# Kernel tuning notes

Hardware: AMD Instinct MI355X
Metric: run time of the kernel (lower is better)

The kernel has to match this reference:

```python
import jax, jax.numpy as jnp
import numpy as np

B, N, H, E, A, V, L = 64, 196, 512, 512, 512, 20000, 20


def setup_inputs() -> dict:
    key = jax.random.key(0)
    ks = jax.random.split(key, 16)
    s = lambda *sh: 0.02
    return {
        "encoder_outputs": jax.random.normal(ks[0], (B, N, H), dtype=jnp.float32),
        "captions": jax.random.randint(ks[1], (B, L), 0, V, dtype=jnp.int64),
        "emb": jax.random.normal(ks[2], (V, E), dtype=jnp.float32) * 0.02,
        "W_ih": jax.random.normal(ks[3], (4 * H, E + H), dtype=jnp.float32) * 0.02,
        "W_hh": jax.random.normal(ks[4], (4 * H, H), dtype=jnp.float32) * 0.02,
        "b_ih": jax.random.normal(ks[5], (4 * H,), dtype=jnp.float32) * 0.02,
        "b_hh": jax.random.normal(ks[6], (4 * H,), dtype=jnp.float32) * 0.02,
        "enc_W": jax.random.normal(ks[7], (A, H), dtype=jnp.float32) * 0.02,
        "enc_b": jax.random.normal(ks[8], (A,), dtype=jnp.float32) * 0.02,
        "dec_W": jax.random.normal(ks[9], (A, H), dtype=jnp.float32) * 0.02,
        "dec_b": jax.random.normal(ks[10], (A,), dtype=jnp.float32) * 0.02,
        "energy_W": jax.random.normal(ks[11], (1, A), dtype=jnp.float32) * 0.02,
        "energy_b": jax.random.normal(ks[12], (1,), dtype=jnp.float32) * 0.02,
        "fc_W": jax.random.normal(ks[13], (V, H), dtype=jnp.float32) * 0.02,
        "fc_b": jax.random.normal(ks[14], (V,), dtype=jnp.float32) * 0.02,
    }


def reference(encoder_outputs, captions, emb, W_ih, W_hh, b_ih, b_hh,
              enc_W, enc_b, dec_W, dec_b, energy_W, energy_b, fc_W, fc_b):
    b, max_len = captions.shape
    hid = W_hh.shape[1]
    vocab = fc_W.shape[0]
    dt = encoder_outputs.dtype

    # encoder projection is hidden-state independent: hoist out of the loop
    enc_proj = jnp.einsum('bnh,ah->bna', encoder_outputs, enc_W) + enc_b  # [B,N,A]
    # teacher forcing ratio = 1.0 => input at step t is captions[:, t-1]
    emb_seq = emb[captions[:, :-1]]                                      # [B,L-1,E]
    emb_seq = jnp.swapaxes(emb_seq, 0, 1)                                # [L-1,B,E]

    def step(carry, x_t):
        h, c = carry
        dec = h @ dec_W.T + dec_b                                        # [B,A]
        scores = jnp.tanh(enc_proj + dec[:, None, :]) @ energy_W[0] + energy_b[0]  # [B,N]
        attw = jax.nn.softmax(scores, axis=1)
        context = jnp.einsum('bn,bnh->bh', attw, encoder_outputs)        # [B,H]
        lstm_in = jnp.concatenate([x_t, context], axis=1)                # [B,E+H]
        gates = lstm_in @ W_ih.T + b_ih + h @ W_hh.T + b_hh              # [B,4H]
        i, f, g, o = jnp.split(gates, 4, axis=1)
        c_new = jax.nn.sigmoid(f) * c + jax.nn.sigmoid(i) * jnp.tanh(g)
        h_new = jax.nn.sigmoid(o) * jnp.tanh(c_new)
        out = h_new @ fc_W.T + fc_b                                      # [B,V]
        return (h_new, c_new), out

    h0 = jnp.zeros((b, hid), dtype=dt)
    c0 = jnp.zeros((b, hid), dtype=dt)
    (_, _), outs = jax.lax.scan(step, (h0, c0), emb_seq)                 # [L-1,B,V]
    outputs = jnp.concatenate(
        [jnp.zeros((b, 1, vocab), dtype=dt), jnp.swapaxes(outs, 0, 1)], axis=1)
    return outputs
```

## Files before the change

kernel.cpp:

```cpp
#include <hip/hip_runtime.h>
#include <hip/hip_bf16.h>
#include <math.h>

#define B   64
#define NN  196
#define HH  512
#define EE  512
#define AA  512
#define VV  20000
#define LL  20

typedef __attribute__((ext_vector_type(8))) short bf16x8;
typedef __attribute__((ext_vector_type(4))) float floatx4;

__device__ __forceinline__ float tanh_fast(float x) {
  float e2 = __expf(2.f * x);
  return 1.f - 2.f / (e2 + 1.f);
}
__device__ __forceinline__ float sigmoid_fast(float x) {
  return 1.f / (1.f + __expf(-x));
}
__device__ __forceinline__ float bf2f(unsigned short u) {
  return __uint_as_float(((unsigned)u) << 16);
}
__device__ __forceinline__ unsigned short f2bf(float v) {
  __hip_bfloat16 h = __float2bfloat16(v);
  return *reinterpret_cast<unsigned short*>(&h);
}

__device__ __forceinline__ int ldsw(int row, int q4) {
  return (row * 4 + (q4 ^ ((row >> 1) & 3))) * 8;
}
__device__ __forceinline__ int ldsw8(int row, int q8) {
  return (row * 8 + (q8 ^ (row & 7))) * 8;
}

__global__ __launch_bounds__(256) void gemm_mfma_bt(
    const unsigned short* __restrict__ Xb, const unsigned short* __restrict__ Wb,
    const float* __restrict__ bias, float* __restrict__ C,
    int M, int N, int K, int lda, int ldC, int outMode, int gridMX) {
  __shared__ unsigned short As[128 * 32];
  __shared__ unsigned short Bs[128 * 32];
  const int tid = threadIdx.x;
  const int lane = tid & 63;
  const int l15 = lane & 15;
  const int q = lane >> 4;
  const int wv = tid >> 6;
  const int wm = (wv >> 1) * 64;
  const int wn = (wv & 1) * 64;
  int mBase, nBase;
  if (gridMX == 2) {
    const int MT = (M + 127) >> 7, NT = (N + 127) >> 7;
    int wg = blockIdx.x;
    int xcd = wg & 7, idx = wg >> 3;
    int kk = idx / MT, mi = idx - kk * MT;
    int p = kk * 8 + xcd;
    if (p >= NT) return;
    mBase = mi * 128;
    nBase = p * 128;
  } else {
    mBase = blockIdx.y * 128;
    nBase = blockIdx.x * 128;
  }

  const int c0 = tid, c1 = tid + 256;
  const int r0 = c0 >> 2, q0 = c0 & 3;
  const int r1 = c1 >> 2, q1 = c1 & 3;
  const int s0 = ldsw(r0, q0), s1 = ldsw(r1, q1);

  floatx4 zero = {0.f, 0.f, 0.f, 0.f};
  floatx4 acc[4][4];
#pragma unroll
  for (int i = 0; i < 4; ++i)
#pragma unroll
    for (int j = 0; j < 4; ++j) acc[i][j] = zero;

  for (int k0 = 0; k0 < K; k0 += 32) {
    uint4 a0 = *(const uint4*)(Xb + (size_t)(mBase + r0) * lda + k0 + q0 * 8);
    uint4 a1 = *(const uint4*)(Xb + (size_t)(mBase + r1) * lda + k0 + q1 * 8);
    uint4 b0 = *(const uint4*)(Wb + (size_t)(nBase + r0) * K + k0 + q0 * 8);
    uint4 b1 = *(const uint4*)(Wb + (size_t)(nBase + r1) * K + k0 + q1 * 8);
    __syncthreads();
    *(uint4*)&As[s0] = a0;
    *(uint4*)&As[s1] = a1;
    *(uint4*)&Bs[s0] = b0;
    *(uint4*)&Bs[s1] = b1;
    __syncthreads();
    bf16x8 af[4], bfv[4];
#pragma unroll
    for (int i = 0; i < 4; ++i)
      af[i] = *(const bf16x8*)&As[ldsw(wm + i * 16 + l15, q)];
#pragma unroll
    for (int j = 0; j < 4; ++j)
      bfv[j] = *(const bf16x8*)&Bs[ldsw(wn + j * 16 + l15, q)];
#pragma unroll
    for (int i = 0; i < 4; ++i)
#pragma unroll
      for (int j = 0; j < 4; ++j)
        acc[i][j] = __builtin_amdgcn_mfma_f32_16x16x32_bf16(af[i], bfv[j],
                                                            acc[i][j], 0, 0, 0);
  }

#pragma unroll
  for (int i = 0; i < 4; ++i) {
#pragma unroll
    for (int j = 0; j < 4; ++j) {
#pragma unroll
      for (int p = 0; p < 4; ++p) {
        int m = mBase + wm + i * 16 + q * 4 + p;
        int n = nBase + wn + j * 16 + l15;
        if (m < M && n < N) {
          float v = acc[i][j][p];
          if (bias) v += bias[n];
          if (outMode == 1) {
            size_t idx = (size_t)(m & 63) * ((size_t)LL * VV) +
                         (size_t)((m >> 6) + 1) * VV + n;
            C[idx] = v;
          } else if (outMode == 2) {
            ((unsigned short*)C)[(size_t)m * ldC + n] = f2bf(v);
          } else {
            C[(size_t)m * ldC + n] = v;
          }
        }
      }
    }
  }
}

__global__ __launch_bounds__(512) void fused_step(
    const unsigned short* __restrict__ enc_projb,
    const unsigned short* __restrict__ encOutb,
    const unsigned short* __restrict__ dec_Wp,
    const float* __restrict__ dec_b, const float* __restrict__ eW,
    const float* __restrict__ eb,
    const unsigned short* __restrict__ Wgi,
    const float* __restrict__ gx,
    float* __restrict__ c,
    unsigned short* __restrict__ xcur,
    unsigned short* __restrict__ xnxt,
    unsigned short* __restrict__ hb_slot,
    int* __restrict__ flags, int target) {
  const int tid = threadIdx.x;

  if (blockIdx.x < 64) {
    const int b = blockIdx.x;
    __shared__ float hs[512];
    __shared__ float sdec[512];
    __shared__ float sw[NN];
    __shared__ float tmp[256];
    __shared__ float cp[1024];

    hs[tid] = bf2f(xcur[(size_t)b * 1024 + tid]);
    __syncthreads();
    {
      float dacc = dec_b[tid];
#pragma unroll 4
      for (int kg = 0; kg < 64; ++kg) {
        bf16x8 w8 = *(const bf16x8*)(dec_Wp + (size_t)((kg << 9) + tid) * 8);
#pragma unroll
        for (int j = 0; j < 8; ++j)
          dacc += hs[kg * 8 + j] * bf2f((unsigned short)w8[j]);
      }
      sdec[tid] = dacc;
    }
    __syncthreads();

    int wvv = tid >> 6, lane = tid & 63;
    float ew8[8], sd8[8];
#pragma unroll
    for (int j = 0; j < 8; ++j) {
      ew8[j] = eW[lane * 8 + j];
      sd8[j] = sdec[lane * 8 + j];
    }
    float eb0 = eb[0];
    for (int n = wvv; n < NN; n += 8) {
      const unsigned short* ep =
          enc_projb + ((size_t)b * NN + n) * 512 + lane * 8;
      bf16x8 v8 = *(const bf16x8*)ep;
      float a = 0.f;
#pragma unroll
      for (int j = 0; j < 8; ++j)
        a += tanh_fast(bf2f((unsigned short)v8[j]) + sd8[j]) * ew8[j];
#pragma unroll
      for (int off = 32; off; off >>= 1) a += __shfl_down(a, off, 64);
      if (lane == 0) sw[n] = a + eb0;
    }
    __syncthreads();

    float v = (tid < NN) ? sw[tid] : -1e30f;
    if (tid < 256) tmp[tid] = v;
    __syncthreads();
    for (int s = 128; s; s >>= 1) {
      if (tid < s) tmp[tid] = fmaxf(tmp[tid], tmp[tid + s]);
      __syncthreads();
    }
    float mx = tmp[0];
    __syncthreads();
    float e = (tid < NN) ? __expf(v - mx) : 0.f;
    if (tid < 256) tmp[tid] = e;
    __syncthreads();
    for (int s = 128; s; s >>= 1) {
      if (tid < s) tmp[tid] += tmp[tid + s];
      __syncthreads();
    }
    float inv = 1.f / tmp[0];
    if (tid < NN) sw[tid] = e * inv;
    __syncthreads();

    int half = tid >> 8, hp = tid & 255;
    const unsigned short* eo = encOutb + (size_t)b * NN * 512 + hp * 2;
    float a0 = 0.f, a1 = 0.f;
    int n0 = half * 98;
#pragma unroll 7
    for (int n = n0; n < n0 + 98; ++n) {
      float w = sw[n];
      unsigned u = *(const unsigned*)(eo + (size_t)n * 512);
      a0 += w * __uint_as_float((u & 0xffffu) << 16);
      a1 += w * __uint_as_float((u >> 16) << 16);
    }
    cp[half * 512 + hp * 2] = a0;
    cp[half * 512 + hp * 2 + 1] = a1;
    __syncthreads();
    xcur[(size_t)b * 1024 + 512 + tid] = f2bf(cp[tid] + cp[512 + tid]);
    __threadfence();
    __syncthreads();
    if (tid == 0)
      __hip_atomic_store(&flags[b], target, __ATOMIC_RELEASE,
                         __HIP_MEMORY_SCOPE_AGENT);
  } else {
    const int nBase = (blockIdx.x - 64) * 128;
    __shared__ unsigned short As[64 * 64];
    __shared__ unsigned short Bs[128 * 64];
    __shared__ float gbuf[64][132];

    const int ar = tid >> 3, aq = tid & 7;
    const int sa = ldsw8(ar, aq);
    const int br0 = tid >> 3, bq0 = tid & 7;
    const int br1 = (tid + 512) >> 3, bq1 = tid & 7;
    const int sb0 = ldsw8(br0, bq0), sb1 = ldsw8(br1, bq1);

    const int lane = tid & 63;
    const int l15 = lane & 15;
    const int q = lane >> 4;
    const int wv = tid >> 6;
    const int wn = (wv & 3) * 32;

    floatx4 zero = {0.f, 0.f, 0.f, 0.f};
    floatx4 acc[4][2];
#pragma unroll
    for (int i = 0; i < 4; ++i)
#pragma unroll
      for (int j = 0; j < 2; ++j) acc[i][j] = zero;

#pragma unroll 1
    for (int ph = 0; ph < 2; ++ph) {
      if (ph == 1) {
        __syncthreads();
        if (tid < 64) {
          while (__hip_atomic_load(&flags[tid], __ATOMIC_ACQUIRE,
                                   __HIP_MEMORY_SCOPE_AGENT) < target)
            __builtin_amdgcn_s_sleep(2);
        }
        __syncthreads();
        __threadfence();
      }
      const int kLo = ph * 512;
#pragma unroll 1
      for (int k0 = kLo; k0 < kLo + 512; k0 += 64) {
        uint4 a0 = *(const uint4*)(xcur + (size_t)ar * 1024 + k0 + aq * 8);
        uint4 b0 =
            *(const uint4*)(Wgi + (size_t)(nBase + br0) * 1024 + k0 + bq0 * 8);
        uint4 b1 =
            *(const uint4*)(Wgi + (size_t)(nBase + br1) * 1024 + k0 + bq1 * 8);
        __syncthreads();
        *(uint4*)&As[sa] = a0;
        *(uint4*)&Bs[sb0] = b0;
        *(uint4*)&Bs[sb1] = b1;
        __syncthreads();
        if (tid < 256) {
#pragma unroll
          for (int ks = 0; ks < 2; ++ks) {
            bf16x8 af[4], bfv[2];
#pragma unroll
            for (int i = 0; i < 4; ++i)
              af[i] = *(const bf16x8*)&As[ldsw8(i * 16 + l15, ks * 4 + q)];
#pragma unroll
            for (int j = 0; j < 2; ++j)
              bfv[j] =
                  *(const bf16x8*)&Bs[ldsw8(wn + j * 16 + l15, ks * 4 + q)];
#pragma unroll
            for (int i = 0; i < 4; ++i)
#pragma unroll
              for (int j = 0; j < 2; ++j)
                acc[i][j] = __builtin_amdgcn_mfma_f32_16x16x32_bf16(
                    af[i], bfv[j], acc[i][j], 0, 0, 0);
          }
        }
      }
    }

    if (tid < 256) {
#pragma unroll
      for (int i = 0; i < 4; ++i)
#pragma unroll
        for (int j = 0; j < 2; ++j)
#pragma unroll
          for (int p = 0; p < 4; ++p)
            gbuf[i * 16 + q * 4 + p][wn + j * 16 + l15] = acc[i][j][p];
    }
    __syncthreads();

#pragma unroll
    for (int it = 0; it < 4; ++it) {
      int e = it * 512 + tid;
      int b = e >> 5, jl = e & 31;
      float4 gv = *(float4*)&gbuf[b][jl * 4];
      float4 gxv = *(const float4*)(gx + (size_t)b * 2048 + nBase + jl * 4);
      float ig = gv.x + gxv.x, fg = gv.y + gxv.y;
      float gg = gv.z + gxv.z, og = gv.w + gxv.w;
      int jg = (nBase >> 2) + jl;
      float cv = c[b * 512 + jg];
      float cn = sigmoid_fast(fg) * cv + sigmoid_fast(ig) * tanh_fast(gg);
      float hn = sigmoid_fast(og) * tanh_fast(cn);
      c[b * 512 + jg] = cn;
      unsigned short hbf = f2bf(hn);
      xnxt[(size_t)b * 1024 + jg] = hbf;
      hb_slot[(size_t)b * 512 + jg] = hbf;
    }
  }
}

#define VB_ENCOUT 2512
#define VB_WGI    4080
#define VB_WB0I   4592
#define VB_ENCW   4848
#define VB_DECW   4912
#define VB_EMB    4976
#define VB_ZOUT   5136
#define VB_CZ     5449
#define VB_XCZ    5457
#define VB_HBPAD  5489
#define VB_BSUM   5493
#define VB_TOTAL  5494

struct PrepArgs {
  const float *fc_W, *enc_out, *W_ih, *W_hh, *b_ih, *b_hh, *enc_W, *dec_W, *emb;
  const int* captions;
  unsigned short *fcWb, *encOutb, *Wgi, *Wb0i, *encWb, *dec_Wp, *embxb, *hb,
      *xcat2;
  float *bsumi, *c, *out;
  int* flags;
};

__global__ __launch_bounds__(256) void prep_all(PrepArgs A) {
  const int tid = threadIdx.x;
  const uint4 z4 = {0u, 0u, 0u, 0u};
  for (int vb = blockIdx.x; vb < VB_TOTAL; vb += gridDim.x) {
    if (vb < VB_ENCOUT) {
      int base = vb * 4096;
#pragma unroll 4
      for (int i = 0; i < 16; ++i) {
        int idx = base + i * 256 + tid;
        int r = idx >> 9, cc = idx & 511;
        float v = (r < 20000) ? A.fc_W[(size_t)r * 512 + cc] : 0.f;
        A.fcWb[idx] = f2bf(v);
      }
    } else if (vb < VB_WGI) {
      int base = (vb - VB_ENCOUT) * 4096;
#pragma unroll 4
      for (int i = 0; i < 16; ++i) {
        int idx = base + i * 256 + tid;
        A.encOutb[idx] = f2bf(A.enc_out[idx]);
      }
    } else if (vb < VB_WB0I) {
      int base = (vb - VB_WGI) * 4096;
#pragma unroll 4
      for (int i = 0; i < 16; ++i) {
        int idx = base + i * 256 + tid;
        int np = idx >> 10, k = idx & 1023;
        int row = (np & 3) * 512 + (np >> 2);
        float v = (k < 512) ? A.W_hh[(size_t)row * 512 + k]
                            : A.W_ih[(size_t)row * 1024 + 512 + (k - 512)];
        A.Wgi[idx] = f2bf(v);
      }
    } else if (vb < VB_ENCW) {
      int base = (vb - VB_WB0I) * 4096;
#pragma unroll 4
      for (int i = 0; i < 16; ++i) {
        int idx = base + i * 256 + tid;
        int np = idx >> 9, k = idx & 511;
        int row = (np & 3) * 512 + (np >> 2);
        A.Wb0i[idx] = f2bf(A.W_ih[(size_t)row * 1024 + k]);
      }
    } else if (vb < VB_DECW) {
      int base = (vb - VB_ENCW) * 4096;
#pragma unroll 4
      for (int i = 0; i < 16; ++i) {
        int idx = base + i * 256 + tid;
        A.encWb[idx] = f2bf(A.enc_W[idx]);
      }
    } else if (vb < VB_EMB) {
      int base = (vb - VB_DECW) * 4096;
#pragma unroll 4
      for (int i = 0; i < 16; ++i) {
        int idx = base + i * 256 + tid;
        int kg = idx >> 12, rem = idx & 4095;
        int a = rem >> 3, j = rem & 7;
        A.dec_Wp[idx] = f2bf(A.dec_W[(size_t)a * 512 + kg * 8 + j]);
      }
    } else if (vb < VB_ZOUT) {
      int base = (vb - VB_EMB) * 4096;
#pragma unroll 4
      for (int i = 0; i < 16; ++i) {
        int idx = base + i * 256 + tid;
        int m = idx >> 9, cc = idx & 511;
        unsigned short r = 0;
        if (m < 1216) {
          int t = m >> 6, b = m & 63;
          int cap = A.captions[b * LL + t];
          r = f2bf(A.emb[(size_t)cap * 512 + cc]);
        }
        A.embxb[idx] = r;
      }
    } else if (vb < VB_CZ) {
      int u0 = (vb - VB_ZOUT) * 1024;
      floatx4 zf = {0.f, 0.f, 0.f, 0.f};
#pragma unroll
      for (int i = 0; i < 4; ++i) {
        int u = u0 + i * 256 + tid;
        if (u < 320000) {
          int b = u / 5000, v4 = u - b * 5000;
          *(floatx4*)(A.out + (size_t)b * ((size_t)LL * VV) + v4 * 4) = zf;
        }
      }
    } else if (vb < VB_XCZ) {
      int u0 = (vb - VB_CZ) * 1024;
      floatx4 zf = {0.f, 0.f, 0.f, 0.f};
#pragma unroll
      for (int i = 0; i < 4; ++i) {
        int u = u0 + i * 256 + tid;
        *(floatx4*)(A.c + (size_t)u * 4) = zf;
      }
    } else if (vb < VB_HBPAD) {
      int u0 = (vb - VB_XCZ) * 1024;
#pragma unroll
      for (int i = 0; i < 4; ++i) {
        int u = u0 + i * 256 + tid;
        ((uint4*)A.xcat2)[u] = z4;
      }
    } else if (vb < VB_BSUM) {
      int u0 = (vb - VB_HBPAD) * 1024;
      uint4* hp = (uint4*)(A.hb + (size_t)1216 * 512);
#pragma unroll
      for (int i = 0; i < 4; ++i) {
        int u = u0 + i * 256 + tid;
        hp[u] = z4;
      }
    } else {
#pragma unroll
      for (int i = 0; i < 8; ++i) {
        int e = i * 256 + tid;
        int row = (e & 3) * 512 + (e >> 2);
        A.bsumi[e] = A.b_ih[row] + A.b_hh[row];
        if (e < 64) A.flags[e] = 0;
      }
    }
  }
}

extern "C" void kernel_launch(void* const* d_in, const int* in_sizes, int n_in,
                              void* d_out, int out_size, void* d_ws, size_t ws_size,
                              hipStream_t stream) {
  const float* enc_out  = (const float*)d_in[0];
  const int*   captions = (const int*)d_in[1];
  const float* emb      = (const float*)d_in[2];
  const float* W_ih     = (const float*)d_in[3];
  const float* W_hh     = (const float*)d_in[4];
  const float* b_ih     = (const float*)d_in[5];
  const float* b_hh     = (const float*)d_in[6];
  const float* enc_W    = (const float*)d_in[7];
  const float* enc_b    = (const float*)d_in[8];
  const float* dec_W    = (const float*)d_in[9];
  const float* dec_b    = (const float*)d_in[10];
  const float* energy_W = (const float*)d_in[11];
  const float* energy_b = (const float*)d_in[12];
  const float* fc_W     = (const float*)d_in[13];
  const float* fc_b     = (const float*)d_in[14];
  float* out = (float*)d_out;

  float* ws = (float*)d_ws;
  float* c          = ws;
  float* gates_all  = c + 32768;
  float* bsumi      = gates_all + (size_t)19 * 131072;
  int*   flags      = (int*)(bsumi + 2048);
  unsigned short* enc_projb = (unsigned short*)(flags + 64);
  unsigned short* fcWb    = enc_projb + (size_t)12544 * 512;
  unsigned short* encWb   = fcWb + (size_t)20096 * 512;
  unsigned short* encOutb = encWb + (size_t)512 * 512;
  unsigned short* Wb0i    = encOutb + (size_t)12544 * 512;
  unsigned short* Wgi     = Wb0i + (size_t)2048 * 512;
  unsigned short* dec_Wp  = Wgi + (size_t)2048 * 1024;
  unsigned short* embxb   = dec_Wp + (size_t)512 * 512;
  unsigned short* hb      = embxb + (size_t)1280 * 512;
  unsigned short* xcat2   = hb + (size_t)1280 * 512;

  PrepArgs pa;
  pa.fc_W = fc_W;     pa.enc_out = enc_out; pa.W_ih = W_ih;  pa.W_hh = W_hh;
  pa.b_ih = b_ih;     pa.b_hh = b_hh;       pa.enc_W = enc_W;
  pa.dec_W = dec_W;   pa.emb = emb;         pa.captions = captions;
  pa.fcWb = fcWb;     pa.encOutb = encOutb; pa.Wgi = Wgi;    pa.Wb0i = Wb0i;
  pa.encWb = encWb;   pa.dec_Wp = dec_Wp;   pa.embxb = embxb;
  pa.hb = hb;         pa.xcat2 = xcat2;     pa.bsumi = bsumi;
  pa.c = c;           pa.out = out;         pa.flags = flags;
  prep_all<<<2560, 256, 0, stream>>>(pa);

  gemm_mfma_bt<<<dim3(16, 10), 256, 0, stream>>>(
      embxb, Wb0i, bsumi, gates_all, 1216, 2048, 512, 512, 2048, 0, 0);

  gemm_mfma_bt<<<dim3(4, 98), 256, 0, stream>>>(
      encOutb, encWb, enc_b, (float*)enc_projb, 12544, 512, 512, 512, 512, 2, 0);

  for (int s = 0; s < LL - 1; ++s) {
    unsigned short* xcur = xcat2 + (size_t)(s & 1) * 131072;
    unsigned short* xnxt = xcat2 + (size_t)((s + 1) & 1) * 131072;
    fused_step<<<80, 512, 0, stream>>>(
        enc_projb, encOutb, dec_Wp, dec_b, energy_W, energy_b, Wgi,
        gates_all + (size_t)s * 131072, c, xcur, xnxt,
        hb + (size_t)s * 32768, flags, s + 1);
  }

  gemm_mfma_bt<<<1600, 256, 0, stream>>>(
      hb, fcWb, fc_b, out, 1216, 20000, 512, 512, 0, 1, 2);
}
```

Measured before the change: 1.550 ms.

## Fuse per-step decoder launches into one persistent kernel with flag barriers

Replaces the 19 per-timestep fused_step launches with a single persistent kernel in which the 64 attention blocks and 16 gate/LSTM blocks loop over timesteps. Cross-step dependencies go through global release/acquire flags (context flags and new h flags) instead of kernel boundaries. This removes per-launch overhead and the implicit grid-wide drain between steps. In exchange it depends on all 80 blocks being co-resident, since spinning waits would otherwise deadlock, and it adds spin-wait latency.

```diff
diff --git a/kernel.cpp b/kernel.cpp
--- a/kernel.cpp
+++ b/kernel.cpp
@@ -127,111 +127,126 @@
   }
 }
 
-__global__ __launch_bounds__(512) void fused_step(
+__global__ __launch_bounds__(512) void decoder_persist(
     const unsigned short* __restrict__ enc_projb,
     const unsigned short* __restrict__ encOutb,
     const unsigned short* __restrict__ dec_Wp,
     const float* __restrict__ dec_b, const float* __restrict__ eW,
     const float* __restrict__ eb,
     const unsigned short* __restrict__ Wgi,
-    const float* __restrict__ gx,
+    const float* __restrict__ gates_all_,
     float* __restrict__ c,
-    unsigned short* __restrict__ xcur,
-    unsigned short* __restrict__ xnxt,
-    unsigned short* __restrict__ hb_slot,
-    int* __restrict__ flags, int target) {
+    unsigned short* __restrict__ xcat2,
+    unsigned short* __restrict__ hb,
+    int* __restrict__ flags) {
   const int tid = threadIdx.x;
+  __shared__ __align__(16) char smem[58368];
+  int* fctx = flags;
+  int* fh = flags + 64;
 
   if (blockIdx.x < 64) {
     const int b = blockIdx.x;
-    __shared__ float hs[512];
-    __shared__ float sdec[512];
-    __shared__ float sw[NN];
-    __shared__ float tmp[256];
-    __shared__ float cp[1024];
-
-    hs[tid] = bf2f(xcur[(size_t)b * 1024 + tid]);
-    __syncthreads();
-    {
-      float dacc = dec_b[tid];
-#pragma unroll 4
-      for (int kg = 0; kg < 64; ++kg) {
-        bf16x8 w8 = *(const bf16x8*)(dec_Wp + (size_t)((kg << 9) + tid) * 8);
+    float* hs = (float*)smem;
+    float* sdec = (float*)(smem + 2048);
+    float* sw = (float*)(smem + 4096);
+    float* tmp = (float*)(smem + 5120);
+    float* cp = (float*)(smem + 6144);
+    const int wvv = tid >> 6, lane = tid & 63;
+    float ew8[8];
+#pragma unroll
+    for (int j = 0; j < 8; ++j) ew8[j] = eW[lane * 8 + j];
+    float eb0 = eb[0];
+    float dbv = dec_b[tid];
+
+    for (int s = 0; s < 19; ++s) {
+      unsigned short* xcur = xcat2 + (size_t)(s & 1) * 131072;
+      if (s > 0) {
+        if (tid < 16) {
+          while (__hip_atomic_load(&fh[tid], __ATOMIC_ACQUIRE,
+                                   __HIP_MEMORY_SCOPE_AGENT) < s)
+            __builtin_amdgcn_s_sleep(2);
+        }
+        __syncthreads();
+      }
+      hs[tid] = bf2f(xcur[(size_t)b * 1024 + tid]);
+      __syncthreads();
+      {
+        float dacc = dbv;
+#pragma unroll 4
+        for (int kg = 0; kg < 64; ++kg) {
+          bf16x8 w8 = *(const bf16x8*)(dec_Wp + (size_t)((kg << 9) + tid) * 8);
+#pragma unroll
+          for (int j = 0; j < 8; ++j)
+            dacc += hs[kg * 8 + j] * bf2f((unsigned short)w8[j]);
+        }
+        sdec[tid] = dacc;
+      }
+      __syncthreads();
+
+      float sd8[8];
+#pragma unroll
+      for (int j = 0; j < 8; ++j) sd8[j] = sdec[lane * 8 + j];
+      for (int n = wvv; n < NN; n += 8) {
+        const unsigned short* ep =
+            enc_projb + ((size_t)b * NN + n) * 512 + lane * 8;
+        bf16x8 v8 = *(const bf16x8*)ep;
+        float a = 0.f;
 #pragma unroll
         for (int j = 0; j < 8; ++j)
-          dacc += hs[kg * 8 + j] * bf2f((unsigned short)w8[j]);
-      }
-      sdec[tid] = dacc;
+          a += tanh_fast(bf2f((unsigned short)v8[j]) + sd8[j]) * ew8[j];
+#pragma unroll
+        for (int off = 32; off; off >>= 1) a += __shfl_down(a, off, 64);
+        if (lane == 0) sw[n] = a + eb0;
+      }
+      __syncthreads();
+
+      float v = (tid < NN) ? sw[tid] : -1e30f;
+      if (tid < 256) tmp[tid] = v;
+      __syncthreads();
+      for (int st = 128; st; st >>= 1) {
+        if (tid < st) tmp[tid] = fmaxf(tmp[tid], tmp[tid + st]);
+        __syncthreads();
+      }
+      float mx = tmp[0];
+      __syncthreads();
+      float e = (tid < NN) ? __expf(v - mx) : 0.f;
+      if (tid < 256) tmp[tid] = e;
+      __syncthreads();
+      for (int st = 128; st; st >>= 1) {
+        if (tid < st) tmp[tid] += tmp[tid + st];
+        __syncthreads();
+      }
+      float inv = 1.f / tmp[0];
+      if (tid < NN) sw[tid] = e * inv;
+      __syncthreads();
+
+      int half = tid >> 8, hp = tid & 255;
+      const unsigned short* eo = encOutb + (size_t)b * NN * 512 + hp * 2;
+      float a0 = 0.f, a1 = 0.f;
+      int n0 = half * 98;
+#pragma unroll 7
+      for (int n = n0; n < n0 + 98; ++n) {
+        float w = sw[n];
+        unsigned u = *(const unsigned*)(eo + (size_t)n * 512);
+        a0 += w * __uint_as_float((u & 0xffffu) << 16);
+        a1 += w * __uint_as_float((u >> 16) << 16);
+      }
+      cp[half * 512 + hp * 2] = a0;
+      cp[half * 512 + hp * 2 + 1] = a1;
+      __syncthreads();
+      xcur[(size_t)b * 1024 + 512 + tid] = f2bf(cp[tid] + cp[512 + tid]);
+      __threadfence();
+      __syncthreads();
+      if (tid == 0)
+        __hip_atomic_store(&fctx[b], s + 1, __ATOMIC_RELEASE,
+                           __HIP_MEMORY_SCOPE_AGENT);
     }
-    __syncthreads();
-
-    int wvv = tid >> 6, lane = tid & 63;
-    float ew8[8], sd8[8];
-#pragma unroll
-    for (int j = 0; j < 8; ++j) {
-      ew8[j] = eW[lane * 8 + j];
-      sd8[j] = sdec[lane * 8 + j];
-    }
-    float eb0 = eb[0];
-    for (int n = wvv; n < NN; n += 8) {
-      const unsigned short* ep =
-          enc_projb + ((size_t)b * NN + n) * 512 + lane * 8;
-      bf16x8 v8 = *(const bf16x8*)ep;
-      float a = 0.f;
-#pragma unroll
-      for (int j = 0; j < 8; ++j)
-        a += tanh_fast(bf2f((unsigned short)v8[j]) + sd8[j]) * ew8[j];
-#pragma unroll
-      for (int off = 32; off; off >>= 1) a += __shfl_down(a, off, 64);
-      if (lane == 0) sw[n] = a + eb0;
-    }
-    __syncthreads();
-
-    float v = (tid < NN) ? sw[tid] : -1e30f;
-    if (tid < 256) tmp[tid] = v;
-    __syncthreads();
-    for (int s = 128; s; s >>= 1) {
-      if (tid < s) tmp[tid] = fmaxf(tmp[tid], tmp[tid + s]);
-      __syncthreads();
-    }
-    float mx = tmp[0];
-    __syncthreads();
-    float e = (tid < NN) ? __expf(v - mx) : 0.f;
-    if (tid < 256) tmp[tid] = e;
-    __syncthreads();
-    for (int s = 128; s; s >>= 1) {
-      if (tid < s) tmp[tid] += tmp[tid + s];
-      __syncthreads();
-    }
-    float inv = 1.f / tmp[0];
-    if (tid < NN) sw[tid] = e * inv;
-    __syncthreads();
-
-    int half = tid >> 8, hp = tid & 255;
-    const unsigned short* eo = encOutb + (size_t)b * NN * 512 + hp * 2;
-    float a0 = 0.f, a1 = 0.f;
-    int n0 = half * 98;
-#pragma unroll 7
-    for (int n = n0; n < n0 + 98; ++n) {
-      float w = sw[n];
-      unsigned u = *(const unsigned*)(eo + (size_t)n * 512);
-      a0 += w * __uint_as_float((u & 0xffffu) << 16);
-      a1 += w * __uint_as_float((u >> 16) << 16);
-    }
-    cp[half * 512 + hp * 2] = a0;
-    cp[half * 512 + hp * 2 + 1] = a1;
-    __syncthreads();
-    xcur[(size_t)b * 1024 + 512 + tid] = f2bf(cp[tid] + cp[512 + tid]);
-    __threadfence();
-    __syncthreads();
-    if (tid == 0)
-      __hip_atomic_store(&flags[b], target, __ATOMIC_RELEASE,
-                         __HIP_MEMORY_SCOPE_AGENT);
   } else {
-    const int nBase = (blockIdx.x - 64) * 128;
-    __shared__ unsigned short As[64 * 64];
-    __shared__ unsigned short Bs[128 * 64];
-    __shared__ float gbuf[64][132];
+    const int g = blockIdx.x - 64;
+    const int nBase = g * 128;
+    unsigned short* As = (unsigned short*)smem;
+    unsigned short* Bs = (unsigned short*)(smem + 8192);
+    float(*gbuf)[132] = (float(*)[132])(smem + 24576);
 
     const int ar = tid >> 3, aq = tid & 7;
     const int sa = ldsw8(ar, aq);
@@ -245,87 +260,108 @@
     const int wv = tid >> 6;
     const int wn = (wv & 3) * 32;
 
-    floatx4 zero = {0.f, 0.f, 0.f, 0.f};
-    floatx4 acc[4][2];
-#pragma unroll
-    for (int i = 0; i < 4; ++i)
-#pragma unroll
-      for (int j = 0; j < 2; ++j) acc[i][j] = zero;
+    for (int s = 0; s < 19; ++s) {
+      unsigned short* xcur = xcat2 + (size_t)(s & 1) * 131072;
+      unsigned short* xnxt = xcat2 + (size_t)((s + 1) & 1) * 131072;
+      const float* gx = gates_all_ + (size_t)s * 131072;
+      unsigned short* hb_slot = hb + (size_t)s * 32768;
+
+      if (s > 0) {
+        if (tid < 16) {
+          while (__hip_atomic_load(&fh[tid], __ATOMIC_ACQUIRE,
+                                   __HIP_MEMORY_SCOPE_AGENT) < s)
+            __builtin_amdgcn_s_sleep(2);
+        }
+        __syncthreads();
+      }
+
+      floatx4 zero = {0.f, 0.f, 0.f, 0.f};
+      floatx4 acc[4][2];
+#pragma unroll
+      for (int i = 0; i < 4; ++i)
+#pragma unroll
+        for (int j = 0; j < 2; ++j) acc[i][j] = zero;
 
 #pragma unroll 1
-    for (int ph = 0; ph < 2; ++ph) {
-      if (ph == 1) {
-        __syncthreads();
-        if (tid < 64) {
-          while (__hip_atomic_load(&flags[tid], __ATOMIC_ACQUIRE,
-                                   __HIP_MEMORY_SCOPE_AGENT) < target)
-            __builtin_amdgcn_s_sleep(2);
-        }
-        __syncthreads();
-        __threadfence();
-      }
-      const int kLo = ph * 512;
+      for (int ph = 0; ph < 2; ++ph) {
+        if (ph == 1) {
+          __syncthreads();
+          if (tid < 64) {
+            while (__hip_atomic_load(&fctx[tid], __ATOMIC_ACQUIRE,
+                                     __HIP_MEMORY_SCOPE_AGENT) < s + 1)
+              __builtin_amdgcn_s_sleep(2);
+          }
+          __syncthreads();
+          __threadfence();
+        }
+        const int kLo = ph * 512;
 #pragma unroll 1
-      for (int k0 = kLo; k0 < kLo + 512; k0 += 64) {
-        uint4 a0 = *(const uint4*)(xcur + (size_t)ar * 1024 + k0 + aq * 8);
-        uint4 b0 =
-            *(const uint4*)(Wgi + (size_t)(nBase + br0) * 1024 + k0 + bq0 * 8);
-        uint4 b1 =
-            *(const uint4*)(Wgi + (size_t)(nBase + br1) * 1024 + k0 + bq1 * 8);
-        __syncthreads();
-        *(uint4*)&As[sa] = a0;
-        *(uint4*)&Bs[sb0] = b0;
-        *(uint4*)&Bs[sb1] = b1;
-        __syncthreads();
-        if (tid < 256) {
-#pragma unroll
-          for (int ks = 0; ks < 2; ++ks) {
-            bf16x8 af[4], bfv[2];
-#pragma unroll
-            for (int i = 0; i < 4; ++i)
-              af[i] = *(const bf16x8*)&As[ldsw8(i * 16 + l15, ks * 4 + q)];
-#pragma unroll
-            for (int j = 0; j < 2; ++j)
-              bfv[j] =
-                  *(const bf16x8*)&Bs[ldsw8(wn + j * 16 + l15, ks * 4 + q)];
-#pragma unroll
-            for (int i = 0; i < 4; ++i)
+        for (int k0 = kLo; k0 < kLo + 512; k0 += 64) {
+          uint4 a0 = *(const uint4*)(xcur + (size_t)ar * 1024 + k0 + aq * 8);
+          uint4 b0 = *(const uint4*)(Wgi + (size_t)(nBase + br0) * 1024 + k0 +
+                                     bq0 * 8);
+          uint4 b1 = *(const uint4*)(Wgi + (size_t)(nBase + br1) * 1024 + k0 +
+                                     bq1 * 8);
+          __syncthreads();
+          *(uint4*)&As[sa] = a0;
+          *(uint4*)&Bs[sb0] = b0;
+          *(uint4*)&Bs[sb1] = b1;
+          __syncthreads();
+          if (tid < 256) {
+#pragma unroll
+            for (int ks = 0; ks < 2; ++ks) {
+              bf16x8 af[4], bfv[2];
+#pragma unroll
+              for (int i = 0; i < 4; ++i)
+                af[i] = *(const bf16x8*)&As[ldsw8(i * 16 + l15, ks * 4 + q)];
 #pragma unroll
               for (int j = 0; j < 2; ++j)
-                acc[i][j] = __builtin_amdgcn_mfma_f32_16x16x32_bf16(
-                    af[i], bfv[j], acc[i][j], 0, 0, 0);
+                bfv[j] =
+                    *(const bf16x8*)&Bs[ldsw8(wn + j * 16 + l15, ks * 4 + q)];
+#pragma unroll
+              for (int i = 0; i < 4; ++i)
+#pragma unroll
+                for (int j = 0; j < 2; ++j)
+                  acc[i][j] = __builtin_amdgcn_mfma_f32_16x16x32_bf16(
+                      af[i], bfv[j], acc[i][j], 0, 0, 0);
+            }
           }
         }
       }
-    }
-
-    if (tid < 256) {
-#pragma unroll
-      for (int i = 0; i < 4; ++i)
-#pragma unroll
-        for (int j = 0; j < 2; ++j)
-#pragma unroll
-          for (int p = 0; p < 4; ++p)
-            gbuf[i * 16 + q * 4 + p][wn + j * 16 + l15] = acc[i][j][p];
-    }
-    __syncthreads();
-
-#pragma unroll
-    for (int it = 0; it < 4; ++it) {
-      int e = it * 512 + tid;
-      int b = e >> 5, jl = e & 31;
-      float4 gv = *(float4*)&gbuf[b][jl * 4];
-      float4 gxv = *(const float4*)(gx + (size_t)b * 2048 + nBase + jl * 4);
-      float ig = gv.x + gxv.x, fg = gv.y + gxv.y;
-      float gg = gv.z + gxv.z, og = gv.w + gxv.w;
-      int jg = (nBase >> 2) + jl;
-      float cv = c[b * 512 + jg];
-      float cn = sigmoid_fast(fg) * cv + sigmoid_fast(ig) * tanh_fast(gg);
-      float hn = sigmoid_fast(og) * tanh_fast(cn);
-      c[b * 512 + jg] = cn;
-      unsigned short hbf = f2bf(hn);
-      xnxt[(size_t)b * 1024 + jg] = hbf;
-      hb_slot[(size_t)b * 512 + jg] = hbf;
+
+      if (tid < 256) {
+#pragma unroll
+        for (int i = 0; i < 4; ++i)
+#pragma unroll
+          for (int j = 0; j < 2; ++j)
+#pragma unroll
+            for (int p = 0; p < 4; ++p)
+              gbuf[i * 16 + q * 4 + p][wn + j * 16 + l15] = acc[i][j][p];
+      }
+      __syncthreads();
+
+#pragma unroll
+      for (int it = 0; it < 4; ++it) {
+        int e = it * 512 + tid;
+        int bb = e >> 5, jl = e & 31;
+        float4 gv = *(float4*)&gbuf[bb][jl * 4];
+        float4 gxv = *(const float4*)(gx + (size_t)bb * 2048 + nBase + jl * 4);
+        float ig = gv.x + gxv.x, fg = gv.y + gxv.y;
+        float gg = gv.z + gxv.z, og = gv.w + gxv.w;
+        int jg = (nBase >> 2) + jl;
+        float cv = c[bb * 512 + jg];
+        float cn = sigmoid_fast(fg) * cv + sigmoid_fast(ig) * tanh_fast(gg);
+        float hn = sigmoid_fast(og) * tanh_fast(cn);
+        c[bb * 512 + jg] = cn;
+        unsigned short hbf = f2bf(hn);
+        xnxt[(size_t)bb * 1024 + jg] = hbf;
+        hb_slot[(size_t)bb * 512 + jg] = hbf;
+      }
+      __threadfence();
+      __syncthreads();
+      if (tid == 0)
+        __hip_atomic_store(&fh[g], s + 1, __ATOMIC_RELEASE,
+                           __HIP_MEMORY_SCOPE_AGENT);
     }
   }
 }
@@ -462,7 +498,7 @@
         int e = i * 256 + tid;
         int row = (e & 3) * 512 + (e >> 2);
         A.bsumi[e] = A.b_ih[row] + A.b_hh[row];
-        if (e < 64) A.flags[e] = 0;
+        if (e < 80) A.flags[e] = 0;
       }
     }
   }
@@ -493,7 +529,7 @@
   float* gates_all  = c + 32768;
   float* bsumi      = gates_all + (size_t)19 * 131072;
   int*   flags      = (int*)(bsumi + 2048);
-  unsigned short* enc_projb = (unsigned short*)(flags + 64);
+  unsigned short* enc_projb = (unsigned short*)(flags + 80);
   unsigned short* fcWb    = enc_projb + (size_t)12544 * 512;
   unsigned short* encWb   = fcWb + (size_t)20096 * 512;
   unsigned short* encOutb = encWb + (size_t)512 * 512;
@@ -520,14 +556,9 @@
   gemm_mfma_bt<<<dim3(4, 98), 256, 0, stream>>>(
       encOutb, encWb, enc_b, (float*)enc_projb, 12544, 512, 512, 512, 512, 2, 0);
 
-  for (int s = 0; s < LL - 1; ++s) {
-    unsigned short* xcur = xcat2 + (size_t)(s & 1) * 131072;
-    unsigned short* xnxt = xcat2 + (size_t)((s + 1) & 1) * 131072;
-    fused_step<<<80, 512, 0, stream>>>(
-        enc_projb, encOutb, dec_Wp, dec_b, energy_W, energy_b, Wgi,
-        gates_all + (size_t)s * 131072, c, xcur, xnxt,
-        hb + (size_t)s * 32768, flags, s + 1);
-  }
+  decoder_persist<<<80, 512, 0, stream>>>(
+      enc_projb, encOutb, dec_Wp, dec_b, energy_W, energy_b, Wgi, gates_all,
+      c, xcat2, hb, flags);
 
   gemm_mfma_bt<<<1600, 256, 0, stream>>>(
       hb, fcWb, fc_b, out, 1216, 20000, 512, 512, 0, 1, 2);
```

Result: slower. 2.014 ms (+29.9%).
